# Kernel optimization log

Hardware: AMD Instinct MI355X
Metric: run time of the kernel (lower is better)

The kernel has to match this reference:

```python
import jax, jax.numpy as jnp
import numpy as np

B, N, DIM = 32, 1024, 512
H, KD, ATTN_RATIO = 8, 64, 4
D = ATTN_RATIO * KD            # value dim per head = 256
DH = D * H                     # 2048
QKV_OUT = DH + 2 * H * KD      # 3072
RES = 32                       # resolution (32, 32), N = 32*32
SCALE = KD ** -0.5


def _make_bias_idxs(res):
    coords = np.stack(np.meshgrid(np.arange(res), np.arange(res), indexing="ij"), -1).reshape(-1, 2)  # [N,2]
    off = np.abs(coords[:, None, :] - coords[None, :, :])  # [N,N,2]
    return jnp.asarray(off[..., 0] * res + off[..., 1], dtype=jnp.int32)  # [N,N] in [0, res*res)


def setup_inputs() -> dict:
    key = jax.random.key(0)
    ks = jax.random.split(key, 6)
    x = jax.random.normal(ks[0], (B, N, DIM), dtype=jnp.float32)
    gamma = jnp.ones((DIM,), jnp.float32)
    beta = jnp.zeros((DIM,), jnp.float32)
    qkv_w = jax.random.normal(ks[1], (DIM, QKV_OUT), jnp.float32) * 0.02
    qkv_b = jnp.zeros((QKV_OUT,), jnp.float32)
    proj_w = jax.random.normal(ks[2], (DH, DIM), jnp.float32) * 0.02
    proj_b = jnp.zeros((DIM,), jnp.float32)
    biases = jax.random.normal(ks[3], (H, RES * RES), jnp.float32) * 0.02
    bias_idxs = _make_bias_idxs(RES)
    return {"x": x, "gamma": gamma, "beta": beta, "qkv_w": qkv_w, "qkv_b": qkv_b,
            "proj_w": proj_w, "proj_b": proj_b, "biases": biases, "bias_idxs": bias_idxs}


def reference(x, gamma, beta, qkv_w, qkv_b, proj_w, proj_b, biases, bias_idxs):
    # LayerNorm
    mu = jnp.mean(x, axis=-1, keepdims=True)
    var = jnp.mean(jnp.square(x - mu), axis=-1, keepdims=True)
    xn = (x - mu) * jax.lax.rsqrt(var + 1e-5) * gamma + beta
    # QKV projection and head split
    qkv = (xn @ qkv_w + qkv_b).reshape(B, N, H, 2 * KD + D)
    q, k, v = jnp.split(qkv, [KD, 2 * KD], axis=-1)  # [B,N,H,KD],[B,N,H,KD],[B,N,H,D]
    # Attention with relative-position bias
    bias = biases[:, bias_idxs]  # [H,N,N]
    attn = jnp.einsum("bqhd,bkhd->bhqk", q, k) * SCALE + bias[None]
    attn = jax.nn.softmax(attn, axis=-1)
    out = jnp.einsum("bhqk,bkhd->bqhd", attn, v).reshape(B, N, DH)
    return out @ proj_w + proj_b
```

## Files before the change

kernel.cpp:

```cpp
#include <hip/hip_runtime.h>
#include <hip/hip_bf16.h>
#include <initializer_list>

typedef _Float16 half8 __attribute__((ext_vector_type(8)));
typedef float floatx4 __attribute__((ext_vector_type(4)));

#define MFMA16(a, b, c) __builtin_amdgcn_mfma_f32_16x16x32_f16((a), (b), (c), 0, 0, 0)

__device__ __forceinline__ void gload16(const void* g, void* l) {
    __builtin_amdgcn_global_load_lds((const __attribute__((address_space(1))) unsigned int*)g,
                                     (__attribute__((address_space(3))) unsigned int*)l,
                                     16, 0, 0);
}

__global__ __launch_bounds__(256) void ln_kernel(const float* __restrict__ x,
                                                 const float* __restrict__ gamma,
                                                 const float* __restrict__ beta,
                                                 _Float16* __restrict__ xn) {
    int row = blockIdx.x;
    int tid = threadIdx.x;
    float2 v = ((const float2*)(x + (size_t)row * 512))[tid];

    __shared__ float red[4];
    __shared__ float mv[2];

    float s = v.x + v.y;
#pragma unroll
    for (int o = 32; o > 0; o >>= 1) s += __shfl_down(s, o);
    if ((tid & 63) == 0) red[tid >> 6] = s;
    __syncthreads();
    if (tid == 0) mv[0] = (red[0] + red[1] + red[2] + red[3]) * (1.f / 512.f);
    __syncthreads();
    float mean = mv[0];

    float dx = v.x - mean, dy = v.y - mean;
    float sq = dx * dx + dy * dy;
#pragma unroll
    for (int o = 32; o > 0; o >>= 1) sq += __shfl_xor(sq, o);
    __syncthreads();
    if ((tid & 63) == 0) red[tid >> 6] = sq;
    __syncthreads();
    if (tid == 0) mv[1] = rsqrtf((red[0] + red[1] + red[2] + red[3]) * (1.f / 512.f) + 1e-5f);
    __syncthreads();
    float rstd = mv[1];

    float g0 = gamma[tid * 2], g1 = gamma[tid * 2 + 1];
    float b0 = beta[tid * 2], b1 = beta[tid * 2 + 1];
    union { _Float16 h[2]; unsigned int u; } pk;
    pk.h[0] = (_Float16)(dx * rstd * g0 + b0);
    pk.h[1] = (_Float16)(dy * rstd * g1 + b1);
    ((unsigned int*)(xn + (size_t)row * 512))[tid] = pk.u;
}

__global__ __launch_bounds__(256) void transpose_cast(const float* __restrict__ in,
                                                      _Float16* __restrict__ out,
                                                      int R, int C) {
    __shared__ float t[32][33];
    int c0 = blockIdx.x * 32, r0 = blockIdx.y * 32;
    int tx = threadIdx.x & 31, ty = threadIdx.x >> 5;
#pragma unroll
    for (int j = 0; j < 4; ++j)
        t[ty + j * 8][tx] = in[(size_t)(r0 + ty + j * 8) * C + c0 + tx];
    __syncthreads();
#pragma unroll
    for (int j = 0; j < 4; ++j)
        out[(size_t)(c0 + ty + j * 8) * R + r0 + tx] = (_Float16)t[tx][ty + j * 8];
}

template <int OUTMODE>
__global__ __launch_bounds__(256) void gemm_bt(const _Float16* __restrict__ A,
                                               const _Float16* __restrict__ Bt,
                                               const float* __restrict__ bias,
                                               void* __restrict__ Cout,
                                               _Float16* __restrict__ Vt,
                                               int M, int N, int K) {
    __shared__ __align__(16) _Float16 Asb[128 * 32];
    __shared__ __align__(16) _Float16 Bsb[128 * 32];

    int m0 = blockIdx.x * 128;
    int n0 = blockIdx.y * 128;
    int tid = threadIdx.x;
    int w = tid >> 6, lane = tid & 63, lrow = lane & 15, quad = lane >> 4;
    int wm = (w >> 1) * 64, wn = (w & 1) * 64;

    int hh = 0, part = 0;
    bool sw = false;
    if (OUTMODE == 2) {
        hh = blockIdx.y / 3;
        part = blockIdx.y - hh * 3;
        sw = (part != 0);
    }

    int srow = lane >> 2;
    int scb = (lane & 3) ^ ((lane >> 3) & 3);
    const _Float16* Abase = A + (size_t)(m0 + w * 16 + srow) * K + scb * 8;
    const _Float16* Bbase = Bt + (size_t)(n0 + w * 16 + srow) * K + scb * 8;
    char* AldsB = (char*)Asb + w * 1024;
    char* BldsB = (char*)Bsb + w * 1024;
    const size_t rowskip = (size_t)64 * K;

    int swz = (lrow >> 1) & 3;

    floatx4 acc[4][4];
#pragma unroll
    for (int i = 0; i < 4; ++i)
#pragma unroll
        for (int j = 0; j < 4; ++j) acc[i][j] = (floatx4){0.f, 0.f, 0.f, 0.f};

    for (int k0 = 0; k0 < K; k0 += 32) {
        __syncthreads();
        gload16(Abase + k0, AldsB);
        gload16(Abase + rowskip + k0, AldsB + 4096);
        gload16(Bbase + k0, BldsB);
        gload16(Bbase + rowskip + k0, BldsB + 4096);
        __syncthreads();

        half8 af[4], bf[4];
#pragma unroll
        for (int i = 0; i < 4; ++i) {
            int r = wm + i * 16 + lrow;
            af[i] = *(const half8*)&Asb[r * 32 + (quad ^ swz) * 8];
        }
#pragma unroll
        for (int j = 0; j < 4; ++j) {
            int r = wn + j * 16 + lrow;
            bf[j] = *(const half8*)&Bsb[r * 32 + (quad ^ swz) * 8];
        }
        if (OUTMODE == 2 && sw) {
#pragma unroll
            for (int i = 0; i < 4; ++i)
#pragma unroll
                for (int j = 0; j < 4; ++j)
                    acc[i][j] = MFMA16(bf[j], af[i], acc[i][j]);
        } else {
#pragma unroll
            for (int i = 0; i < 4; ++i)
#pragma unroll
                for (int j = 0; j < 4; ++j)
                    acc[i][j] = MFMA16(af[i], bf[j], acc[i][j]);
        }
    }

    if (OUTMODE == 2 && sw) {
        int b_rel = m0 >> 10;
        int tok0 = (m0 & 1023) + wm;
        _Float16* vbase = Vt + (((size_t)b_rel * 8 + hh) * 256 + (part - 1) * 128) * 1024;
#pragma unroll
        for (int j = 0; j < 4; ++j)
#pragma unroll
            for (int r = 0; r < 4; ++r) {
                int d = wn + j * 16 + quad * 4 + r;
                float bv = bias[n0 + d];
                _Float16* vrow = vbase + (size_t)d * 1024 + tok0;
#pragma unroll
                for (int i = 0; i < 4; ++i)
                    vrow[i * 16 + lrow] = (_Float16)(acc[i][j][r] + bv);
            }
        return;
    }

#pragma unroll
    for (int i = 0; i < 4; ++i)
#pragma unroll
        for (int j = 0; j < 4; ++j) {
            int colg = n0 + wn + j * 16 + lrow;
            int coll = wn + j * 16 + lrow;
            float bv = bias[colg];
#pragma unroll
            for (int r = 0; r < 4; ++r) {
                int rowg = m0 + wm + i * 16 + quad * 4 + r;
                float v = acc[i][j][r] + bv;
                if (OUTMODE == 1) {
                    ((float*)Cout)[(size_t)rowg * N + colg] = v;
                } else {
                    ((_Float16*)Cout)[(size_t)rowg * 1024 + hh * 128 + coll] = (_Float16)v;
                }
            }
        }
}

__global__ __launch_bounds__(256) void attn_kernel(const _Float16* __restrict__ qk,
                                                   const _Float16* __restrict__ vt,
                                                   const float* __restrict__ biases,
                                                   _Float16* __restrict__ out) {
    int h  = blockIdx.x;
    int qt = blockIdx.y;
    int b  = blockIdx.z;

    int tid = threadIdx.x;
    int w = tid >> 6, lane = tid & 63, lrow = lane & 15, quad = lane >> 4;

    __shared__ float bias_lds[1024];
    __shared__ __align__(16) _Float16 K_lds[2][32 * 72];
    __shared__ __align__(16) _Float16 V_s[2][256 * 32];

    for (int i = tid; i < 1024; i += 256) bias_lds[i] = biases[h * 1024 + i];

    int q0 = qt * 128 + w * 32 + lrow;
    const _Float16* qb = qk + ((size_t)(b * 1024 + q0)) * 1024 + h * 128;
    half8 aq[2][2];
    aq[0][0] = *(const half8*)(qb + quad * 8);
    aq[0][1] = *(const half8*)(qb + 32 + quad * 8);
    aq[1][0] = *(const half8*)(qb + 16 * 1024 + quad * 8);
    aq[1][1] = *(const half8*)(qb + 16 * 1024 + 32 + quad * 8);

    int key_l = tid >> 3, kd8 = (tid & 7) * 8;
    const _Float16* ksrc = qk + ((size_t)(b * 1024 + key_l)) * 1024 + h * 128 + 64 + kd8;
    int cc = tid & 3;
    const _Float16* vsrc0 = vt + ((size_t)((b * 8 + h) * 256 + (tid >> 2))) * 1024 + cc * 4;

    int qr = qt * 4 + w;

    float m_[2] = {-1e30f, -1e30f}, l_[2] = {0.f, 0.f};
    floatx4 od[2][16];
#pragma unroll
    for (int f = 0; f < 2; ++f)
#pragma unroll
        for (int dt = 0; dt < 16; ++dt) od[f][dt] = (floatx4){0.f, 0.f, 0.f, 0.f};

    uint4 kreg;
    uint2 vA[4], vB[4];

#define LOADT(t)                                                          \
    do {                                                                  \
        kreg = *(const uint4*)(ksrc + (size_t)(t) * 32 * 1024);           \
        const _Float16* vp = vsrc0 + (size_t)(t) * 32;                    \
        _Pragma("unroll") for (int it = 0; it < 4; ++it) {                \
            const _Float16* p = vp + (size_t)it * 64 * 1024;              \
            vA[it] = *(const uint2*)p;                                    \
            vB[it] = *(const uint2*)(p + 16);                             \
        }                                                                 \
    } while (0)

#define WRITET(bb)                                                        \
    do {                                                                  \
        *(uint4*)&K_lds[bb][key_l * 72 + kd8] = kreg;                     \
        _Pragma("unroll") for (int it = 0; it < 4; ++it) {                \
            uint4 v;                                                      \
            v.x = vA[it].x; v.y = vA[it].y; v.z = vB[it].x; v.w = vB[it].y; \
            *(uint4*)&V_s[bb][((tid >> 2) + it * 64) * 32 + cc * 8] = v;  \
        }                                                                 \
    } while (0)

    LOADT(0);
    WRITET(0);
    LOADT(1);
    __syncthreads();

    for (int kt = 0; kt < 32; ++kt) {
        int bufc = kt & 1;
        const _Float16* Kc = K_lds[bufc];
        const _Float16* Vc = V_s[bufc];

        floatx4 sc[2][2];
#pragma unroll
        for (int f = 0; f < 2; ++f)
#pragma unroll
            for (int t = 0; t < 2; ++t) sc[f][t] = (floatx4){0.f, 0.f, 0.f, 0.f};
        {
            half8 kf00 = *(const half8*)&Kc[lrow * 72 + quad * 8];
            half8 kf01 = *(const half8*)&Kc[lrow * 72 + 32 + quad * 8];
            half8 kf10 = *(const half8*)&Kc[(16 + lrow) * 72 + quad * 8];
            half8 kf11 = *(const half8*)&Kc[(16 + lrow) * 72 + 32 + quad * 8];
#pragma unroll
            for (int f = 0; f < 2; ++f) {
                sc[f][0] = MFMA16(kf00, aq[f][0], sc[f][0]);
                sc[f][0] = MFMA16(kf01, aq[f][1], sc[f][0]);
                sc[f][1] = MFMA16(kf10, aq[f][0], sc[f][1]);
                sc[f][1] = MFMA16(kf11, aq[f][1], sc[f][1]);
            }
        }

        int rowoff = abs(qr - kt) << 5;
        union H8 { _Float16 hh[8]; half8 v; } pa[2];

#pragma unroll
        for (int f = 0; f < 2; ++f) {
            int qcf = lrow + f * 16;
            float s_[8];
#pragma unroll
            for (int t = 0; t < 2; ++t)
#pragma unroll
                for (int r = 0; r < 4; ++r) {
                    int kc = t * 16 + quad * 4 + r;
                    s_[t * 4 + r] = sc[f][t][r] * 0.125f + bias_lds[rowoff + abs(qcf - kc)];
                }

            float pmax = fmaxf(fmaxf(fmaxf(s_[0], s_[1]), fmaxf(s_[2], s_[3])),
                               fmaxf(fmaxf(s_[4], s_[5]), fmaxf(s_[6], s_[7])));
            pmax = fmaxf(pmax, __shfl_xor(pmax, 16));
            pmax = fmaxf(pmax, __shfl_xor(pmax, 32));

            if (!__all(pmax - m_[f] <= 8.f)) {
                float mnew = fmaxf(m_[f], pmax);
                float alpha = __expf(m_[f] - mnew);
                m_[f] = mnew;
                l_[f] *= alpha;
                float a4[4];
#pragma unroll
                for (int r = 0; r < 4; ++r) a4[r] = __shfl(alpha, quad * 4 + r, 16);
#pragma unroll
                for (int dt = 0; dt < 16; ++dt)
#pragma unroll
                    for (int r = 0; r < 4; ++r) od[f][dt][r] *= a4[r];
            }

            float rs = 0.f;
#pragma unroll
            for (int i = 0; i < 8; ++i) {
                float p = __expf(s_[i] - m_[f]);
                pa[f].hh[i] = (_Float16)p;
                rs += p;
            }
            rs += __shfl_xor(rs, 16);
            rs += __shfl_xor(rs, 32);
            l_[f] += rs;
        }

        if (kt < 31) WRITET(bufc ^ 1);
        if (kt < 30) LOADT(kt + 2);

#pragma unroll
        for (int dt = 0; dt < 16; ++dt) {
            half8 bv = *(const half8*)&Vc[(dt * 16 + lrow) * 32 + quad * 8];
            od[0][dt] = MFMA16(pa[0].v, bv, od[0][dt]);
            od[1][dt] = MFMA16(pa[1].v, bv, od[1][dt]);
        }
        __syncthreads();
    }
#undef LOADT
#undef WRITET

#pragma unroll
    for (int f = 0; f < 2; ++f)
#pragma unroll
        for (int r = 0; r < 4; ++r) {
            float lq = __shfl(l_[f], quad * 4 + r, 16);
            float inv = 1.f / lq;
            int qg = qt * 128 + w * 32 + f * 16 + quad * 4 + r;
            _Float16* orow = out + ((size_t)(b * 1024 + qg)) * 2048 + h * 256;
#pragma unroll
            for (int dt = 0; dt < 16; ++dt)
                orow[dt * 16 + lrow] = (_Float16)(od[f][dt][r] * inv);
        }
}

extern "C" void kernel_launch(void* const* d_in, const int* in_sizes, int n_in,
                              void* d_out, int out_size, void* d_ws, size_t ws_size,
                              hipStream_t stream) {
    const float* x      = (const float*)d_in[0];
    const float* gamma  = (const float*)d_in[1];
    const float* beta   = (const float*)d_in[2];
    const float* qkv_w  = (const float*)d_in[3];
    const float* qkv_b  = (const float*)d_in[4];
    const float* proj_w = (const float*)d_in[5];
    const float* proj_b = (const float*)d_in[6];
    const float* biases = (const float*)d_in[7];

    float* out = (float*)d_out;

    _Float16* ws      = (_Float16*)d_ws;
    _Float16* qkv_wt  = ws;
    _Float16* proj_wt = qkv_wt + (size_t)512 * 3072;
    _Float16* xn      = proj_wt + (size_t)2048 * 512;
    _Float16* chunk0  = xn + (size_t)32768 * 512;

    const size_t FIXED_HALVES = (size_t)512 * 3072 + (size_t)2048 * 512 + (size_t)32768 * 512;
    int CB = 0;
    for (int cb : {16, 8, 4, 2, 1}) {
        size_t halves = FIXED_HALVES + (size_t)cb * 1024 * (1024 + 2048 + 2048);
        if (halves * sizeof(_Float16) <= ws_size) { CB = cb; break; }
    }
    if (CB == 0) return;
    _Float16* qk_c  = chunk0;
    _Float16* vt_c  = qk_c + (size_t)CB * 1024 * 1024;
    _Float16* att_c = vt_c + (size_t)CB * 1024 * 2048;

    transpose_cast<<<dim3(3072 / 32, 512 / 32), 256, 0, stream>>>(qkv_w, qkv_wt, 512, 3072);
    transpose_cast<<<dim3(512 / 32, 2048 / 32), 256, 0, stream>>>(proj_w, proj_wt, 2048, 512);
    ln_kernel<<<32768, 256, 0, stream>>>(x, gamma, beta, xn);

    const int MC = CB * 1024;
    for (int c = 0; c < 32 / CB; ++c) {
        const _Float16* xn_c = xn + (size_t)c * MC * 512;
        gemm_bt<2><<<dim3(MC / 128, 24), 256, 0, stream>>>(xn_c, qkv_wt, qkv_b,
                                                           (void*)qk_c, vt_c, MC, 3072, 512);
        attn_kernel<<<dim3(8, 8, CB), 256, 0, stream>>>(qk_c, vt_c, biases, att_c);
        float* out_c = out + (size_t)c * MC * 512;
        gemm_bt<1><<<dim3(MC / 128, 4), 256, 0, stream>>>(att_c, proj_wt, proj_b,
                                                          (void*)out_c, nullptr, MC, 512, 2048);
    }
}
```

Baseline: 836.3 us.

## Stage attention K/V tiles with direct global-to-LDS loads and XOR swizzle

Replaces the register-staged K/V prefetch (global load into registers, then an LDS write) with direct global_load_lds 16-byte transfers into a double buffer, issued one tile ahead at the top of each iteration. The K tile drops its padding in favour of an XOR swizzle to avoid bank conflicts, and the V-transpose writer in the QKV GEMM is changed to a permuted token order that matches the new per-lane V load layout. Launch bounds now request 3 blocks per CU. This cuts register pressure and VGPR-to-LDS write instructions, but the tighter register cap risks spills, and correctness depends on the permuted V layout matching between the producer and consumer kernels.

```diff
diff --git a/kernel.cpp b/kernel.cpp
--- a/kernel.cpp
+++ b/kernel.cpp
@@ -145,6 +145,7 @@
         int b_rel = m0 >> 10;
         int tok0 = (m0 & 1023) + wm;
         _Float16* vbase = Vt + (((size_t)b_rel * 8 + hh) * 256 + (part - 1) * 128) * 1024;
+        int poff0 = ((lrow >> 2) << 3) + (lrow & 3);
 #pragma unroll
         for (int j = 0; j < 4; ++j)
 #pragma unroll
@@ -154,7 +155,7 @@
                 _Float16* vrow = vbase + (size_t)d * 1024 + tok0;
 #pragma unroll
                 for (int i = 0; i < 4; ++i)
-                    vrow[i * 16 + lrow] = (_Float16)(acc[i][j][r] + bv);
+                    vrow[(i >> 1) * 32 + ((i & 1) << 2) + poff0] = (_Float16)(acc[i][j][r] + bv);
             }
         return;
     }
@@ -179,10 +180,10 @@
         }
 }
 
-__global__ __launch_bounds__(256) void attn_kernel(const _Float16* __restrict__ qk,
-                                                   const _Float16* __restrict__ vt,
-                                                   const float* __restrict__ biases,
-                                                   _Float16* __restrict__ out) {
+__global__ __launch_bounds__(256, 3) void attn_kernel(const _Float16* __restrict__ qk,
+                                                      const _Float16* __restrict__ vt,
+                                                      const float* __restrict__ biases,
+                                                      _Float16* __restrict__ out) {
     int h  = blockIdx.x;
     int qt = blockIdx.y;
     int b  = blockIdx.z;
@@ -191,7 +192,7 @@
     int w = tid >> 6, lane = tid & 63, lrow = lane & 15, quad = lane >> 4;
 
     __shared__ float bias_lds[1024];
-    __shared__ __align__(16) _Float16 K_lds[2][32 * 72];
+    __shared__ __align__(16) _Float16 K_lds[2][32 * 64];
     __shared__ __align__(16) _Float16 V_s[2][256 * 32];
 
     for (int i = tid; i < 1024; i += 256) bias_lds[i] = biases[h * 1024 + i];
@@ -204,10 +205,12 @@
     aq[1][0] = *(const half8*)(qb + 16 * 1024 + quad * 8);
     aq[1][1] = *(const half8*)(qb + 16 * 1024 + 32 + quad * 8);
 
-    int key_l = tid >> 3, kd8 = (tid & 7) * 8;
-    const _Float16* ksrc = qk + ((size_t)(b * 1024 + key_l)) * 1024 + h * 128 + 64 + kd8;
-    int cc = tid & 3;
-    const _Float16* vsrc0 = vt + ((size_t)((b * 8 + h) * 256 + (tid >> 2))) * 1024 + cc * 4;
+    int kswz = (lane & 7) ^ ((lane >> 3) & 7);
+    const _Float16* ksrc_g = qk + ((size_t)(b * 1024 + w * 8 + (lane >> 3))) * 1024 + h * 128 + 64 + kswz * 8;
+    const _Float16* vsrc_g = vt + ((size_t)((b * 8 + h) * 256 + w * 64 + (lane >> 2))) * 1024 + (lane & 3) * 8;
+
+    int koff0 = lrow * 64 + ((quad) ^ (lrow & 7)) * 8;
+    int koff1 = lrow * 64 + ((4 + quad) ^ (lrow & 7)) * 8;
 
     int qr = qt * 4 + w;
 
@@ -218,33 +221,16 @@
 #pragma unroll
         for (int dt = 0; dt < 16; ++dt) od[f][dt] = (floatx4){0.f, 0.f, 0.f, 0.f};
 
-    uint4 kreg;
-    uint2 vA[4], vB[4];
-
-#define LOADT(t)                                                          \
-    do {                                                                  \
-        kreg = *(const uint4*)(ksrc + (size_t)(t) * 32 * 1024);           \
-        const _Float16* vp = vsrc0 + (size_t)(t) * 32;                    \
-        _Pragma("unroll") for (int it = 0; it < 4; ++it) {                \
-            const _Float16* p = vp + (size_t)it * 64 * 1024;              \
-            vA[it] = *(const uint2*)p;                                    \
-            vB[it] = *(const uint2*)(p + 16);                             \
-        }                                                                 \
+#define STAGE(t)                                                                  \
+    do {                                                                          \
+        int bb_ = (t) & 1;                                                        \
+        gload16(ksrc_g + (size_t)(t) * 32 * 1024, &K_lds[bb_][w * 8 * 64]);       \
+        _Pragma("unroll") for (int it = 0; it < 4; ++it)                          \
+            gload16(vsrc_g + (size_t)it * 16 * 1024 + (t) * 32,                   \
+                    &V_s[bb_][(w * 64 + it * 16) * 32]);                          \
     } while (0)
 
-#define WRITET(bb)                                                        \
-    do {                                                                  \
-        *(uint4*)&K_lds[bb][key_l * 72 + kd8] = kreg;                     \
-        _Pragma("unroll") for (int it = 0; it < 4; ++it) {                \
-            uint4 v;                                                      \
-            v.x = vA[it].x; v.y = vA[it].y; v.z = vB[it].x; v.w = vB[it].y; \
-            *(uint4*)&V_s[bb][((tid >> 2) + it * 64) * 32 + cc * 8] = v;  \
-        }                                                                 \
-    } while (0)
-
-    LOADT(0);
-    WRITET(0);
-    LOADT(1);
+    STAGE(0);
     __syncthreads();
 
     for (int kt = 0; kt < 32; ++kt) {
@@ -252,23 +238,26 @@
         const _Float16* Kc = K_lds[bufc];
         const _Float16* Vc = V_s[bufc];
 
+        if (kt < 31) STAGE(kt + 1);
+
         floatx4 sc[2][2];
 #pragma unroll
         for (int f = 0; f < 2; ++f)
 #pragma unroll
             for (int t = 0; t < 2; ++t) sc[f][t] = (floatx4){0.f, 0.f, 0.f, 0.f};
         {
-            half8 kf00 = *(const half8*)&Kc[lrow * 72 + quad * 8];
-            half8 kf01 = *(const half8*)&Kc[lrow * 72 + 32 + quad * 8];
-            half8 kf10 = *(const half8*)&Kc[(16 + lrow) * 72 + quad * 8];
-            half8 kf11 = *(const half8*)&Kc[(16 + lrow) * 72 + 32 + quad * 8];
-#pragma unroll
-            for (int f = 0; f < 2; ++f) {
-                sc[f][0] = MFMA16(kf00, aq[f][0], sc[f][0]);
-                sc[f][0] = MFMA16(kf01, aq[f][1], sc[f][0]);
-                sc[f][1] = MFMA16(kf10, aq[f][0], sc[f][1]);
-                sc[f][1] = MFMA16(kf11, aq[f][1], sc[f][1]);
-            }
+            half8 ka = *(const half8*)&Kc[koff0];
+            half8 kb = *(const half8*)&Kc[koff1];
+            sc[0][0] = MFMA16(ka, aq[0][0], sc[0][0]);
+            sc[0][0] = MFMA16(kb, aq[0][1], sc[0][0]);
+            sc[1][0] = MFMA16(ka, aq[1][0], sc[1][0]);
+            sc[1][0] = MFMA16(kb, aq[1][1], sc[1][0]);
+            ka = *(const half8*)&Kc[16 * 64 + koff0];
+            kb = *(const half8*)&Kc[16 * 64 + koff1];
+            sc[0][1] = MFMA16(ka, aq[0][0], sc[0][1]);
+            sc[0][1] = MFMA16(kb, aq[0][1], sc[0][1]);
+            sc[1][1] = MFMA16(ka, aq[1][0], sc[1][1]);
+            sc[1][1] = MFMA16(kb, aq[1][1], sc[1][1]);
         }
 
         int rowoff = abs(qr - kt) << 5;
@@ -317,9 +306,6 @@
             l_[f] += rs;
         }
 
-        if (kt < 31) WRITET(bufc ^ 1);
-        if (kt < 30) LOADT(kt + 2);
-
 #pragma unroll
         for (int dt = 0; dt < 16; ++dt) {
             half8 bv = *(const half8*)&Vc[(dt * 16 + lrow) * 32 + quad * 8];
@@ -328,8 +314,7 @@
         }
         __syncthreads();
     }
-#undef LOADT
-#undef WRITET
+#undef STAGE
 
 #pragma unroll
     for (int f = 0; f < 2; ++f)
```

Result: slower. 1.220 ms (+45.9%).
